# Kernel optimization log

Hardware: AMD Instinct MI355X
Metric: run time of the kernel (lower is better)

Reference implementation:

```python
import jax, jax.numpy as jnp
import numpy as np

N_NODES = 50000
N_EDGES = 800000
IN_CH, HID_CH, OUT_CH = 128, 128, 64


def gcn_conv(x, edge_index, edge_weight, W, b, n_nodes):
    """PyG GCNConv: h = D^-1/2 (A + I) D^-1/2 (x @ W) + b, with weighted edges."""
    src, dst = edge_index[0], edge_index[1]
    loop = jnp.arange(n_nodes)
    src_l = jnp.concatenate([src, loop])               # [E+N]
    dst_l = jnp.concatenate([dst, loop])               # [E+N]
    w_l = jnp.concatenate([edge_weight, jnp.ones((n_nodes,), x.dtype)])
    deg = jax.ops.segment_sum(w_l, dst_l, num_segments=n_nodes)  # weighted in-degree incl. self-loop
    dinv = jnp.where(deg > 0, jax.lax.rsqrt(deg), 0.0)
    norm = dinv[src_l] * w_l * dinv[dst_l]             # [E+N]
    h = x @ W                                          # [N, out]
    msg = h[src_l] * norm[:, None]                     # [E+N, out] gather + scale
    out = jax.ops.segment_sum(msg, dst_l, num_segments=n_nodes)  # scatter-add
    return out + b


def setup_inputs() -> dict:
    key = jax.random.key(0)
    k = jax.random.split(key, 8)
    x = jax.random.normal(k[0], (N_NODES, IN_CH), dtype=jnp.float32)
    edge_index = jax.random.randint(k[1], (2, N_EDGES), 0, N_NODES, dtype=jnp.int64)
    edge_weight = jax.random.uniform(k[2], (N_EDGES,), dtype=jnp.float32)
    s1 = 1.0 / np.sqrt(IN_CH)
    s2 = 1.0 / np.sqrt(HID_CH)
    W1 = jax.random.uniform(k[3], (IN_CH, HID_CH), jnp.float32, -s1, s1)
    b1 = jnp.zeros((HID_CH,), jnp.float32)
    W2 = jax.random.uniform(k[4], (HID_CH, OUT_CH), jnp.float32, -s2, s2)
    b2 = jnp.zeros((OUT_CH,), jnp.float32)
    return {"x": x, "edge_index": edge_index, "edge_weight": edge_weight,
            "W1": W1, "b1": b1, "W2": W2, "b2": b2}


def reference(x, edge_index, edge_weight, W1, b1, W2, b2):
    n = x.shape[0]
    h = jax.nn.relu(gcn_conv(x, edge_index, edge_weight, W1, b1, n))
    # dropout(p=0.5) is identity in eval mode
    h = gcn_conv(h, edge_index, edge_weight, W2, b2, n)
    return jax.nn.log_softmax(h, axis=1)
```

## Files before the change

### kernel.cpp

```cpp
#include <hip/hip_runtime.h>
#include <math.h>

static constexpr int CH_IN  = 128;
static constexpr int CH_HID = 128;
static constexpr int CH_OUT = 64;
static constexpr int NBLK1  = 256;

typedef __attribute__((ext_vector_type(8))) short bf16x8;
typedef __attribute__((ext_vector_type(4))) float f32x4;


__device__ __forceinline__ unsigned short f2bf(float f) {
    unsigned int u = __float_as_uint(f);
    u = (u + 0x7fffu + ((u >> 16) & 1u)) >> 16;
    return (unsigned short)u;
}
__device__ __forceinline__ unsigned int pack2(float lo, float hi) {
    return (unsigned int)f2bf(lo) | ((unsigned int)f2bf(hi) << 16);
}
__device__ __forceinline__ void unpack2(unsigned int u, float& lo, float& hi) {
    lo = __uint_as_float(u << 16);
    hi = __uint_as_float(u & 0xffff0000u);
}
__device__ __forceinline__ unsigned int relu2(unsigned int u) {
    unsigned int m = 0;
    if (!(u & 0x8000u)) m |= 0xffffu;
    if (!(u & 0x80000000u)) m |= 0xffff0000u;
    return u & m;
}

__device__ __forceinline__ void gacc8(const uint2* __restrict__ hp, int stride, int s,
                                      int ci, float nm, float* acc) {
    uint2 v = hp[(size_t)s * stride + ci];
    int x = (int)v.x, y = (int)v.y;
    acc[0] = fmaf((float)(char)(x      ), nm, acc[0]);
    acc[1] = fmaf((float)(char)(x >>  8), nm, acc[1]);
    acc[2] = fmaf((float)(char)(x >> 16), nm, acc[2]);
    acc[3] = fmaf((float)(x >> 24),       nm, acc[3]);
    acc[4] = fmaf((float)(char)(y      ), nm, acc[4]);
    acc[5] = fmaf((float)(char)(y >>  8), nm, acc[5]);
    acc[6] = fmaf((float)(char)(y >> 16), nm, acc[6]);
    acc[7] = fmaf((float)(y >> 24),       nm, acc[7]);
}

__device__ __forceinline__ void unq8(uint2 v, float sc, float* hn) {
    int x = (int)v.x, y = (int)v.y;
    hn[0] = (float)(char)(x      ) * sc; hn[1] = (float)(char)(x >>  8) * sc;
    hn[2] = (float)(char)(x >> 16) * sc; hn[3] = (float)(x >> 24)       * sc;
    hn[4] = (float)(char)(y      ) * sc; hn[5] = (float)(char)(y >>  8) * sc;
    hn[6] = (float)(char)(y >> 16) * sc; hn[7] = (float)(y >> 24)       * sc;
}

__device__ __forceinline__ int block_incl_scan_256(int v, int lane, int wid) {
    __shared__ int wtot[4];
    int s = v;
    #pragma unroll
    for (int off = 1; off < 64; off <<= 1) {
        int t = __shfl_up(s, off, 64);
        if (lane >= off) s += t;
    }
    if (lane == 63) wtot[wid] = s;
    __syncthreads();
    int woff = 0;
    for (int j = 0; j < wid; ++j) woff += wtot[j];
    return s + woff;
}


__device__ __forceinline__ void gemm128q_body(const float* __restrict__ X,
                                              const unsigned short* __restrict__ Wt,
                                              signed char* __restrict__ Hq,
                                              float* __restrict__ scl, int N, int blk) {
    constexpr int NCT = CH_HID / 16;
    __shared__ unsigned short As[64 * 136];
    const int tid = threadIdx.x;
    const int lane = tid & 63, wv = tid >> 6;
    const int row0 = blk * 64;

    #pragma unroll
    for (int j = 0; j < 8; ++j) {
        int f = j * 256 + tid;
        int row = f >> 5, col = (f & 31) * 4;
        float4 v = make_float4(0.f, 0.f, 0.f, 0.f);
        if (row0 + row < N)
            v = *reinterpret_cast<const float4*>(X + (size_t)(row0 + row) * CH_IN + col);
        uint2 p;
        p.x = pack2(v.x, v.y);
        p.y = pack2(v.z, v.w);
        *reinterpret_cast<uint2*>(&As[row * 136 + col]) = p;
    }
    __syncthreads();

    const int rw0  = wv * 16;
    const int arow = rw0 + (lane & 15);
    const int kgrp = (lane >> 4) * 8;
    f32x4 acc[NCT];
    #pragma unroll
    for (int c = 0; c < NCT; ++c) acc[c] = f32x4{0.f, 0.f, 0.f, 0.f};

    #pragma unroll
    for (int kk = 0; kk < 4; ++kk) {
        bf16x8 af = *reinterpret_cast<const bf16x8*>(&As[arow * 136 + kk * 32 + kgrp]);
        #pragma unroll
        for (int ct = 0; ct < NCT; ++ct) {
            bf16x8 bf = *reinterpret_cast<const bf16x8*>(
                Wt + (size_t)(ct * 16 + (lane & 15)) * 128 + kk * 32 + kgrp);
            acc[ct] = __builtin_amdgcn_mfma_f32_16x16x32_bf16(af, bf, acc[ct], 0, 0, 0);
        }
    }

    const int orow0 = row0 + rw0 + (lane >> 4) * 4;
    const int ocol  = lane & 15;
    #pragma unroll
    for (int r = 0; r < 4; ++r) {
        float m = 0.f;
        #pragma unroll
        for (int ct = 0; ct < NCT; ++ct) m = fmaxf(m, fabsf(acc[ct][r]));
        m = fmaxf(m, __shfl_xor(m, 1, 64));
        m = fmaxf(m, __shfl_xor(m, 2, 64));
        m = fmaxf(m, __shfl_xor(m, 4, 64));
        m = fmaxf(m, __shfl_xor(m, 8, 64));
        int row = orow0 + r;
        float inv = (m > 0.f) ? 127.f / m : 0.f;
        if (row < N) {
            if (ocol == 0) scl[row] = (m > 0.f) ? m / 127.f : 0.f;
            #pragma unroll
            for (int ct = 0; ct < NCT; ++ct)
                Hq[(size_t)row * CH_HID + ct * 16 + ocol] =
                    (signed char)__float2int_rn(acc[ct][r] * inv);
        }
    }
}


__global__ void k_count(const int* __restrict__ ei, int* __restrict__ cnt_bk,
                        int E, int nbk, int epb,
                        const float* __restrict__ W1, unsigned short* __restrict__ w1t,
                        const float* __restrict__ W2, unsigned short* __restrict__ w2t) {
    __shared__ int bcnt[256];
    const int tid = threadIdx.x;
    if ((int)blockIdx.x < NBLK1) {
        const int b = blockIdx.x;
        bcnt[tid] = 0;
        __syncthreads();
        const int e0 = b * epb, e1 = min(E, e0 + epb);
        for (int e = e0 + tid; e < e1; e += 256)
            atomicAdd(&bcnt[ei[E + e] >> 8], 1);
        __syncthreads();
        if (tid < nbk) cnt_bk[tid * NBLK1 + b] = bcnt[tid];
    } else {
        int j = (blockIdx.x - NBLK1) * 256 + tid;
        if (j < CH_HID * 128) {
            int c = j >> 7, k = j & 127;
            w1t[(size_t)c * 128 + k] = f2bf(W1[(size_t)k * CH_HID + c]);
            return;
        }
        j -= CH_HID * 128;
        if (j < CH_OUT * 128) {
            int c = j >> 7, k = j & 127;
            w2t[(size_t)c * 128 + k] = f2bf(W2[(size_t)k * CH_OUT + c]);
        }
    }
}


__global__ void k_bscan(const int* __restrict__ cnt_bk, int* __restrict__ off_bk,
                        int* __restrict__ btot) {
    const int k = blockIdx.x, tid = threadIdx.x, lane = tid & 63, wid = tid >> 6;
    int c = cnt_bk[k * NBLK1 + tid];
    int incl = block_incl_scan_256(c, lane, wid);
    off_bk[k * NBLK1 + tid] = incl - c;
    if (tid == 255) btot[k] = incl;
}


__global__ void __launch_bounds__(256) k_fat(
        const float* __restrict__ x, const unsigned short* __restrict__ w1t,
        signed char* __restrict__ h1q, float* __restrict__ scl1, int N, int nbg,
        const int* __restrict__ ei, const float* __restrict__ w,
        const int* __restrict__ btot, const int* __restrict__ off_bk,
        uint2* __restrict__ ebuck, int E, int nbk, int epb) {
    if ((int)blockIdx.x < nbg) {
        gemm128q_body(x, w1t, h1q, scl1, N, blockIdx.x);
    } else {
        __shared__ int lcur[256];
        const int b = blockIdx.x - nbg;
        const int tid = threadIdx.x, lane = tid & 63, wid = tid >> 6;
        int v = (tid < nbk) ? btot[tid] : 0;
        int incl = block_incl_scan_256(v, lane, wid);
        if (tid < nbk) lcur[tid] = (incl - v) + off_bk[tid * NBLK1 + b];
        __syncthreads();
        const int e0 = b * epb, e1 = min(E, e0 + epb);
        for (int e = e0 + tid; e < e1; e += 256) {
            unsigned int s = (unsigned int)ei[e];
            unsigned int d = (unsigned int)ei[E + e];
            int pos = atomicAdd(&lcur[d >> 8], 1);
            ebuck[pos] = make_uint2((d << 16) | s, __float_as_uint(w[e]));
        }
    }
}


__global__ void __launch_bounds__(256) k_gemm2(const unsigned short* __restrict__ X,
        const unsigned short* __restrict__ Wt, signed char* __restrict__ Hq,
        float* __restrict__ scl, int N) {
    constexpr int COLS = CH_OUT, NCT = COLS / 16;
    __shared__ unsigned short As[64 * 136];
    const int tid = threadIdx.x;
    const int lane = tid & 63, wv = tid >> 6;
    const int row0 = blockIdx.x * 64;

    #pragma unroll
    for (int j = 0; j < 4; ++j) {
        int f = j * 256 + tid;
        int row = f >> 4, col = (f & 15) * 8;
        uint4 v = make_uint4(0u, 0u, 0u, 0u);
        if (row0 + row < N) {
            v = *reinterpret_cast<const uint4*>(X + (size_t)(row0 + row) * CH_IN + col);
            v.x = relu2(v.x); v.y = relu2(v.y);
            v.z = relu2(v.z); v.w = relu2(v.w);
        }
        *reinterpret_cast<uint4*>(&As[row * 136 + col]) = v;
    }
    __syncthreads();

    const int rw0  = wv * 16;
    const int arow = rw0 + (lane & 15);
    const int kgrp = (lane >> 4) * 8;
    f32x4 acc[NCT];
    #pragma unroll
    for (int c = 0; c < NCT; ++c) acc[c] = f32x4{0.f, 0.f, 0.f, 0.f};

    #pragma unroll
    for (int kk = 0; kk < 4; ++kk) {
        bf16x8 af = *reinterpret_cast<const bf16x8*>(&As[arow * 136 + kk * 32 + kgrp]);
        #pragma unroll
        for (int ct = 0; ct < NCT; ++ct) {
            bf16x8 bf = *reinterpret_cast<const bf16x8*>(
                Wt + (size_t)(ct * 16 + (lane & 15)) * 128 + kk * 32 + kgrp);
            acc[ct] = __builtin_amdgcn_mfma_f32_16x16x32_bf16(af, bf, acc[ct], 0, 0, 0);
        }
    }

    const int orow0 = row0 + rw0 + (lane >> 4) * 4;
    const int ocol  = lane & 15;
    #pragma unroll
    for (int r = 0; r < 4; ++r) {
        float m = 0.f;
        #pragma unroll
        for (int ct = 0; ct < NCT; ++ct) m = fmaxf(m, fabsf(acc[ct][r]));
        m = fmaxf(m, __shfl_xor(m, 1, 64));
        m = fmaxf(m, __shfl_xor(m, 2, 64));
        m = fmaxf(m, __shfl_xor(m, 4, 64));
        m = fmaxf(m, __shfl_xor(m, 8, 64));
        int row = orow0 + r;
        float inv = (m > 0.f) ? 127.f / m : 0.f;
        if (row < N) {
            if (ocol == 0) scl[row] = (m > 0.f) ? m / 127.f : 0.f;
            #pragma unroll
            for (int ct = 0; ct < NCT; ++ct)
                Hq[(size_t)row * COLS + ct * 16 + ocol] =
                    (signed char)__float2int_rn(acc[ct][r] * inv);
        }
    }
}


__global__ void k_csr(const uint2* __restrict__ ebuck, const int* __restrict__ btot,
                      int* __restrict__ rowptr, float* __restrict__ dinv,
                      int2* __restrict__ epack, int N, int nbk) {
    __shared__ int ncnt[256];
    __shared__ float wsm[256];
    __shared__ int ebeg_s, eend_s;
    const int k = blockIdx.x, tid = threadIdx.x, lane = tid & 63, wid = tid >> 6;
    int v = (tid < nbk) ? btot[tid] : 0;
    int incl0 = block_incl_scan_256(v, lane, wid);
    if (tid == k) { ebeg_s = incl0 - v; eend_s = incl0; }
    ncnt[tid] = 0; wsm[tid] = 0.f;
    __syncthreads();
    const int ebeg = ebeg_s, eend = eend_s;
    for (int i = ebeg + tid; i < eend; i += 256) {
        uint2 p = ebuck[i];
        int dl = (p.x >> 16) & 255;
        atomicAdd(&ncnt[dl], 1);
        atomicAdd(&wsm[dl], __uint_as_float(p.y));
    }
    __syncthreads();
    int c = ncnt[tid];
    int incl = block_incl_scan_256(c, lane, wid);
    const int nd = k * 256 + tid;
    if (nd < N) {
        rowptr[nd + 1] = ebeg + incl;
        dinv[nd] = rsqrtf(1.0f + wsm[tid]);
    }
    if (k == 0 && tid == 0) rowptr[0] = 0;
    __syncthreads();
    ncnt[tid] = ebeg + incl - c;
    __syncthreads();
    for (int i = ebeg + tid; i < eend; i += 256) {
        uint2 p = ebuck[i];
        int dl = (p.x >> 16) & 255;
        int pos = atomicAdd(&ncnt[dl], 1);
        epack[pos] = make_int2((int)(p.x & 0xFFFFu), (int)p.y);
    }
}


__global__ void k_agg128(const int* __restrict__ rowptr, const int2* __restrict__ epack,
                         const float* __restrict__ dinv, const float* __restrict__ scl,
                         const signed char* __restrict__ hq,
                         const float* __restrict__ b, unsigned short* __restrict__ out, int N) {
    const int node = (blockIdx.x * blockDim.x + threadIdx.x) >> 6;
    const int lane = threadIdx.x & 63;
    if (node >= N) return;
    const int beg = rowptr[node], end = rowptr[node + 1];
    const float dd = dinv[node];
    const int g  = lane >> 4;
    const int ci = lane & 15;
    const uint2* hp = (const uint2*)hq;

    float acc[8];
    #pragma unroll
    for (int q = 0; q < 8; ++q) acc[q] = 0.f;

    for (int i0 = beg; i0 < end; i0 += 64) {
        const int m = min(64, end - i0);
        int s_l = 0; float nm_l = 0.f;
        if (lane < m) {
            int2 p = epack[i0 + lane];
            s_l = p.x;
            nm_l = __int_as_float(p.y) * dinv[p.x] * scl[p.x];
        }
        int j = 0;
        for (; j + 16 <= m; j += 16) {
            #pragma unroll
            for (int kk = 0; kk < 4; ++kk) {
                int idx = j + 4 * kk + g;
                int   s  = __shfl(s_l, idx, 64);
                float nm = __shfl(nm_l, idx, 64);
                gacc8(hp, 16, s, ci, nm, acc);
            }
        }
        for (; j < m; j += 4) {
            int idx = j + g;
            int   s  = __shfl(s_l, idx, 64);
            float nm = __shfl(nm_l, idx, 64);
            gacc8(hp, 16, s, ci, nm, acc);
        }
    }
    #pragma unroll
    for (int q = 0; q < 8; ++q) {
        acc[q] += __shfl_xor(acc[q], 16, 64);
        acc[q] += __shfl_xor(acc[q], 32, 64);
    }
    float hn[8];
    unq8(hp[(size_t)node * 16 + ci], scl[node], hn);
    float4 b0 = *reinterpret_cast<const float4*>(b + 8 * ci);
    float4 b1v = *reinterpret_cast<const float4*>(b + 8 * ci + 4);
    const float bb[8] = {b0.x, b0.y, b0.z, b0.w, b1v.x, b1v.y, b1v.z, b1v.w};
    float res[8];
    #pragma unroll
    for (int q = 0; q < 8; ++q)
        res[q] = fmaf(acc[q], dd, fmaf(hn[q], dd * dd, bb[q]));
    if (g == 0) {
        uint4 o;
        o.x = pack2(res[0], res[1]); o.y = pack2(res[2], res[3]);
        o.z = pack2(res[4], res[5]); o.w = pack2(res[6], res[7]);
        ((uint4*)out)[(size_t)node * 16 + ci] = o;
    }
}


__global__ void k_agg64(const int* __restrict__ rowptr, const int2* __restrict__ epack,
                        const float* __restrict__ dinv, const float* __restrict__ scl,
                        const signed char* __restrict__ hq,
                        const float* __restrict__ b, float* __restrict__ out, int N) {
    const int node = (blockIdx.x * blockDim.x + threadIdx.x) >> 6;
    const int lane = threadIdx.x & 63;
    if (node >= N) return;
    const int beg = rowptr[node], end = rowptr[node + 1];
    const float dd = dinv[node];
    const int g  = lane >> 3;
    const int ci = lane & 7;
    const uint2* hp = (const uint2*)hq;

    float acc[8];
    #pragma unroll
    for (int q = 0; q < 8; ++q) acc[q] = 0.f;

    for (int i0 = beg; i0 < end; i0 += 64) {
        const int m = min(64, end - i0);
        int s_l = 0; float nm_l = 0.f;
        if (lane < m) {
            int2 p = epack[i0 + lane];
            s_l = p.x;
            nm_l = __int_as_float(p.y) * dinv[p.x] * scl[p.x];
        }
        int j = 0;
        for (; j + 32 <= m; j += 32) {
            #pragma unroll
            for (int kk = 0; kk < 4; ++kk) {
                int idx = j + 8 * kk + g;
                int   s  = __shfl(s_l, idx, 64);
                float nm = __shfl(nm_l, idx, 64);
                gacc8(hp, 8, s, ci, nm, acc);
            }
        }
        for (; j < m; j += 8) {
            int idx = j + g;
            int   s  = __shfl(s_l, idx, 64);
            float nm = __shfl(nm_l, idx, 64);
            gacc8(hp, 8, s, ci, nm, acc);
        }
    }
    #pragma unroll
    for (int q = 0; q < 8; ++q) {
        acc[q] += __shfl_xor(acc[q], 8, 64);
        acc[q] += __shfl_xor(acc[q], 16, 64);
        acc[q] += __shfl_xor(acc[q], 32, 64);
    }
    float hn[8];
    unq8(hp[(size_t)node * 8 + ci], scl[node], hn);
    float4 b0 = *reinterpret_cast<const float4*>(b + 8 * ci);
    float4 b1v = *reinterpret_cast<const float4*>(b + 8 * ci + 4);
    const float bb[8] = {b0.x, b0.y, b0.z, b0.w, b1v.x, b1v.y, b1v.z, b1v.w};
    float res[8];
    #pragma unroll
    for (int q = 0; q < 8; ++q)
        res[q] = fmaf(acc[q], dd, fmaf(hn[q], dd * dd, bb[q]));

    float mx = res[0];
    #pragma unroll
    for (int q = 1; q < 8; ++q) mx = fmaxf(mx, res[q]);
    mx = fmaxf(mx, __shfl_xor(mx, 1, 64));
    mx = fmaxf(mx, __shfl_xor(mx, 2, 64));
    mx = fmaxf(mx, __shfl_xor(mx, 4, 64));
    float sm = 0.f;
    #pragma unroll
    for (int q = 0; q < 8; ++q) sm += expf(res[q] - mx);
    sm += __shfl_xor(sm, 1, 64);
    sm += __shfl_xor(sm, 2, 64);
    sm += __shfl_xor(sm, 4, 64);
    float lse = mx + logf(sm);
    if (g == 0) {
        float4 o0 = make_float4(res[0] - lse, res[1] - lse, res[2] - lse, res[3] - lse);
        float4 o1 = make_float4(res[4] - lse, res[5] - lse, res[6] - lse, res[7] - lse);
        *reinterpret_cast<float4*>(out + (size_t)node * 64 + 8 * ci)     = o0;
        *reinterpret_cast<float4*>(out + (size_t)node * 64 + 8 * ci + 4) = o1;
    }
}

extern "C" void kernel_launch(void* const* d_in, const int* in_sizes, int n_in,
                              void* d_out, int out_size, void* d_ws, size_t ws_size,
                              hipStream_t stream) {
    const float* x  = (const float*)d_in[0];
    const int*   ei = (const int*)d_in[1];
    const float* w  = (const float*)d_in[2];
    const float* W1 = (const float*)d_in[3];
    const float* b1 = (const float*)d_in[4];
    const float* W2 = (const float*)d_in[5];
    const float* b2 = (const float*)d_in[6];
    float* out = (float*)d_out;

    const int N = in_sizes[0] / CH_IN;
    const int E = in_sizes[2];
    const int NBK = (N + 255) >> 8;
    const int EPB = (E + NBLK1 - 1) / NBLK1;
    const int WTB = (CH_HID * 128 + CH_OUT * 128 + 255) / 256;

    float* ws0   = (float*)d_ws;
    float* ws    = ws0;
    float* dinv  = ws;               ws += N;
    float* scl1  = ws;               ws += N;
    float* scl2  = ws;               ws += N;
    int*   rowptr= (int*)ws;         ws += (N + 2);
    int*   cnt_bk= (int*)ws;         ws += 256 * NBLK1;
    int*   off_bk= (int*)ws;         ws += 256 * NBLK1;
    int*   btot  = (int*)ws;         ws += 256;
    uint2* ebuck = (uint2*)ws;       ws += (size_t)2 * E;
    int2*  epack = (int2*)ws;        ws += (size_t)2 * E;
    { size_t off = (size_t)(ws - ws0) & 3; if (off) ws += 4 - off; }
    unsigned short* w1t  = (unsigned short*)ws;  ws += (size_t)CH_HID * 128 / 2;
    unsigned short* w2t  = (unsigned short*)ws;  ws += (size_t)CH_OUT * 128 / 2;
    signed char*    h1q  = (signed char*)ws;     ws += (size_t)N * CH_HID / 4;
    unsigned short* out1 = (unsigned short*)ws;  ws += (size_t)N * CH_HID / 2;
    signed char*    h2q  = (signed char*)ws;     ws += (size_t)N * CH_OUT / 4;

    const int B = 256;

    k_count<<<NBLK1 + WTB, B, 0, stream>>>(ei, cnt_bk, E, NBK, EPB, W1, w1t, W2, w2t);

    k_bscan<<<NBK, 256, 0, stream>>>(cnt_bk, off_bk, btot);

    {
        const int nbg = (N + 63) / 64;
        k_fat<<<nbg + NBLK1, B, 0, stream>>>(x, w1t, h1q, scl1, N, nbg,
                                             ei, w, btot, off_bk, ebuck, E, NBK, EPB);
    }

    k_csr<<<NBK, 256, 0, stream>>>(ebuck, btot, rowptr, dinv, epack, N, NBK);

    k_agg128<<<(N * 64 + B - 1) / B, B, 0, stream>>>(rowptr, epack, dinv, scl1, h1q, b1, out1, N);

    k_gemm2<<<(N + 63) / 64, 256, 0, stream>>>(out1, w2t, h2q, scl2, N);

    k_agg64<<<(N * 64 + B - 1) / B, B, 0, stream>>>(rowptr, epack, dinv, scl2, h2q, b2, out, N);
}
```

Baseline: 127.3 us.

## Split layer-1 aggregation across two waves per node with 16-byte gathers

k_agg128 now assigns two wavefronts per node, each covering half of the 128 int8 channels. Each lane gathers a 16-byte uint4 chunk (16 channels) instead of 8 bytes, and 16 edges are processed in parallel per wave. The aim is more parallelism per node and wider loads to hide gather latency. In exchange, each wave re-reads the edge list and source dinv/scl values, and it needs 16 accumulators and two extra cross-lane reduction steps.

```diff
diff --git a/kernel.cpp b/kernel.cpp
--- a/kernel.cpp
+++ b/kernel.cpp
@@ -43,12 +43,46 @@
     acc[7] = fmaf((float)(y >> 24),       nm, acc[7]);
 }
 
+__device__ __forceinline__ void gacc16(const uint4* __restrict__ hp, int stride, int s,
+                                       int chunk, float nm, float* acc) {
+    uint4 v = hp[(size_t)s * stride + chunk];
+    int a = (int)v.x, bq = (int)v.y, c = (int)v.z, d = (int)v.w;
+    acc[ 0] = fmaf((float)(char)(a       ), nm, acc[ 0]);
+    acc[ 1] = fmaf((float)(char)(a  >>  8), nm, acc[ 1]);
+    acc[ 2] = fmaf((float)(char)(a  >> 16), nm, acc[ 2]);
+    acc[ 3] = fmaf((float)(a  >> 24),       nm, acc[ 3]);
+    acc[ 4] = fmaf((float)(char)(bq      ), nm, acc[ 4]);
+    acc[ 5] = fmaf((float)(char)(bq >>  8), nm, acc[ 5]);
+    acc[ 6] = fmaf((float)(char)(bq >> 16), nm, acc[ 6]);
+    acc[ 7] = fmaf((float)(bq >> 24),       nm, acc[ 7]);
+    acc[ 8] = fmaf((float)(char)(c       ), nm, acc[ 8]);
+    acc[ 9] = fmaf((float)(char)(c  >>  8), nm, acc[ 9]);
+    acc[10] = fmaf((float)(char)(c  >> 16), nm, acc[10]);
+    acc[11] = fmaf((float)(c  >> 24),       nm, acc[11]);
+    acc[12] = fmaf((float)(char)(d       ), nm, acc[12]);
+    acc[13] = fmaf((float)(char)(d  >>  8), nm, acc[13]);
+    acc[14] = fmaf((float)(char)(d  >> 16), nm, acc[14]);
+    acc[15] = fmaf((float)(d  >> 24),       nm, acc[15]);
+}
+
 __device__ __forceinline__ void unq8(uint2 v, float sc, float* hn) {
     int x = (int)v.x, y = (int)v.y;
     hn[0] = (float)(char)(x      ) * sc; hn[1] = (float)(char)(x >>  8) * sc;
     hn[2] = (float)(char)(x >> 16) * sc; hn[3] = (float)(x >> 24)       * sc;
     hn[4] = (float)(char)(y      ) * sc; hn[5] = (float)(char)(y >>  8) * sc;
     hn[6] = (float)(char)(y >> 16) * sc; hn[7] = (float)(y >> 24)       * sc;
+}
+
+__device__ __forceinline__ void unq16(uint4 v, float sc, float* hn) {
+    int a = (int)v.x, bq = (int)v.y, c = (int)v.z, d = (int)v.w;
+    hn[ 0] = (float)(char)(a       ) * sc; hn[ 1] = (float)(char)(a  >>  8) * sc;
+    hn[ 2] = (float)(char)(a  >> 16) * sc; hn[ 3] = (float)(a  >> 24)       * sc;
+    hn[ 4] = (float)(char)(bq      ) * sc; hn[ 5] = (float)(char)(bq >>  8) * sc;
+    hn[ 6] = (float)(char)(bq >> 16) * sc; hn[ 7] = (float)(bq >> 24)       * sc;
+    hn[ 8] = (float)(char)(c       ) * sc; hn[ 9] = (float)(char)(c  >>  8) * sc;
+    hn[10] = (float)(char)(c  >> 16) * sc; hn[11] = (float)(c  >> 24)       * sc;
+    hn[12] = (float)(char)(d       ) * sc; hn[13] = (float)(char)(d  >>  8) * sc;
+    hn[14] = (float)(char)(d  >> 16) * sc; hn[15] = (float)(d  >> 24)       * sc;
 }
 
 __device__ __forceinline__ int block_incl_scan_256(int v, int lane, int wid) {
@@ -310,18 +344,21 @@
                          const float* __restrict__ dinv, const float* __restrict__ scl,
                          const signed char* __restrict__ hq,
                          const float* __restrict__ b, unsigned short* __restrict__ out, int N) {
-    const int node = (blockIdx.x * blockDim.x + threadIdx.x) >> 6;
+    const int gw   = (blockIdx.x * blockDim.x + threadIdx.x) >> 6;
+    const int node = gw >> 1;
+    const int half = gw & 1;
     const int lane = threadIdx.x & 63;
     if (node >= N) return;
     const int beg = rowptr[node], end = rowptr[node + 1];
     const float dd = dinv[node];
-    const int g  = lane >> 4;
-    const int ci = lane & 15;
-    const uint2* hp = (const uint2*)hq;
-
-    float acc[8];
-    #pragma unroll
-    for (int q = 0; q < 8; ++q) acc[q] = 0.f;
+    const int g  = lane >> 2;
+    const int ci = lane & 3;
+    const int chunk = half * 4 + ci;
+    const uint4* hp = (const uint4*)hq;
+
+    float acc[16];
+    #pragma unroll
+    for (int q = 0; q < 16; ++q) acc[q] = 0.f;
 
     for (int i0 = beg; i0 < end; i0 += 64) {
         const int m = min(64, end - i0);
@@ -332,41 +369,46 @@
             nm_l = __int_as_float(p.y) * dinv[p.x] * scl[p.x];
         }
         int j = 0;
-        for (; j + 16 <= m; j += 16) {
+        if (m == 64) {
             #pragma unroll
             for (int kk = 0; kk < 4; ++kk) {
-                int idx = j + 4 * kk + g;
+                int idx = 16 * kk + g;
                 int   s  = __shfl(s_l, idx, 64);
                 float nm = __shfl(nm_l, idx, 64);
-                gacc8(hp, 16, s, ci, nm, acc);
+                gacc16(hp, 8, s, chunk, nm, acc);
             }
-        }
-        for (; j < m; j += 4) {
+            j = 64;
+        }
+        for (; j < m; j += 16) {
             int idx = j + g;
             int   s  = __shfl(s_l, idx, 64);
             float nm = __shfl(nm_l, idx, 64);
-            gacc8(hp, 16, s, ci, nm, acc);
-        }
-    }
-    #pragma unroll
-    for (int q = 0; q < 8; ++q) {
+            gacc16(hp, 8, s, chunk, nm, acc);
+        }
+    }
+    #pragma unroll
+    for (int q = 0; q < 16; ++q) {
+        acc[q] += __shfl_xor(acc[q], 4, 64);
+        acc[q] += __shfl_xor(acc[q], 8, 64);
         acc[q] += __shfl_xor(acc[q], 16, 64);
         acc[q] += __shfl_xor(acc[q], 32, 64);
     }
-    float hn[8];
-    unq8(hp[(size_t)node * 16 + ci], scl[node], hn);
-    float4 b0 = *reinterpret_cast<const float4*>(b + 8 * ci);
-    float4 b1v = *reinterpret_cast<const float4*>(b + 8 * ci + 4);
-    const float bb[8] = {b0.x, b0.y, b0.z, b0.w, b1v.x, b1v.y, b1v.z, b1v.w};
-    float res[8];
-    #pragma unroll
-    for (int q = 0; q < 8; ++q)
-        res[q] = fmaf(acc[q], dd, fmaf(hn[q], dd * dd, bb[q]));
+    float hn[16];
+    unq16(hp[(size_t)node * 8 + chunk], scl[node], hn);
+    const float* bp = b + half * 64 + ci * 16;
+    float res[16];
+    #pragma unroll
+    for (int q = 0; q < 16; ++q)
+        res[q] = fmaf(acc[q], dd, fmaf(hn[q], dd * dd, bp[q]));
     if (g == 0) {
-        uint4 o;
-        o.x = pack2(res[0], res[1]); o.y = pack2(res[2], res[3]);
-        o.z = pack2(res[4], res[5]); o.w = pack2(res[6], res[7]);
-        ((uint4*)out)[(size_t)node * 16 + ci] = o;
+        unsigned int* ob = (unsigned int*)out + (size_t)node * 64 + half * 32 + ci * 8;
+        uint4 o0, o1;
+        o0.x = pack2(res[0],  res[1]);  o0.y = pack2(res[2],  res[3]);
+        o0.z = pack2(res[4],  res[5]);  o0.w = pack2(res[6],  res[7]);
+        o1.x = pack2(res[8],  res[9]);  o1.y = pack2(res[10], res[11]);
+        o1.z = pack2(res[12], res[13]); o1.w = pack2(res[14], res[15]);
+        *reinterpret_cast<uint4*>(ob)     = o0;
+        *reinterpret_cast<uint4*>(ob + 4) = o1;
     }
 }
 
@@ -500,7 +542,10 @@
 
     k_csr<<<NBK, 256, 0, stream>>>(ebuck, btot, rowptr, dinv, epack, N, NBK);
 
-    k_agg128<<<(N * 64 + B - 1) / B, B, 0, stream>>>(rowptr, epack, dinv, scl1, h1q, b1, out1, N);
+    {
+        const size_t waves = (size_t)N * 2;
+        k_agg128<<<(waves * 64 + B - 1) / B, B, 0, stream>>>(rowptr, epack, dinv, scl1, h1q, b1, out1, N);
+    }
 
     k_gemm2<<<(N + 63) / 64, 256, 0, stream>>>(out1, w2t, h2q, scl2, N);
 
```

Result: slower. 168.6 us (+32.5%).
